# Kernel optimization log

Hardware: AMD Instinct MI355X
Metric: run time of the kernel (lower is better)

## Reference

```python
import jax, jax.numpy as jnp
import numpy as np

B, H, S, D = 2, 16, 2048, 64
DEGREE = 2
EPS = 1e-4


def setup_inputs() -> dict:
    key = jax.random.key(0)
    kq, kk, kv = jax.random.split(key, 3)
    q = jax.random.normal(kq, (B, H, S, D), dtype=jnp.float32)
    k = jax.random.normal(kk, (B, H, S, D), dtype=jnp.float32)
    v = jax.random.normal(kv, (B, H, S, D), dtype=jnp.float32)
    return {"q": q, "k": k, "v": v}


def reference(q, k, v):
    # dots: [B,H,S,S] = QK^T
    dots = jnp.einsum("bhsd,bhtd->bhst", q, k)
    # polynomial kernel: x^degree, row-normalized with clamped denom
    x = dots ** DEGREE
    denom = jnp.maximum(x.sum(axis=-1, keepdims=True), EPS)
    attn = x / denom
    # weighted V sum: [B,H,S,D]
    return jnp.einsum("bhst,bhtd->bhsd", attn, v)
```

## Files before the change

### kernel.cpp

```cpp
#include <hip/hip_runtime.h>


#define S_LEN 2048
#define DH    64
#define BQ    64
#define BK    64
#define EPSTR 68
#define PSTR  65
#define BH_N  32
#define PER_BH (S_LEN * DH)
#define NT    (S_LEN / BK)

typedef __bf16 bf16x8 __attribute__((ext_vector_type(8)));
typedef __bf16 bf16x2 __attribute__((ext_vector_type(2)));
typedef float  f32x4  __attribute__((ext_vector_type(4)));
typedef float  f32x16 __attribute__((ext_vector_type(16)));
typedef unsigned int uivec2 __attribute__((ext_vector_type(2)));

__device__ __forceinline__ unsigned short f2bf(float f) {
    union { float f; unsigned int u; } x; x.f = f;
    unsigned int u = x.u;
    return (unsigned short)((u + 0x7fffu + ((u >> 16) & 1u)) >> 16);
}

__device__ __forceinline__ unsigned int pack2bf(float lo, float hi) {
#if __has_builtin(__builtin_amdgcn_cvt_pk_bf16_f32)
    bf16x2 p = __builtin_amdgcn_cvt_pk_bf16_f32(lo, hi);
    union { bf16x2 v; unsigned int u; } c; c.v = p;
    return c.u;
#else
    return (unsigned int)f2bf(lo) | ((unsigned int)f2bf(hi) << 16);
#endif
}

__device__ __forceinline__ void pl32swap(unsigned int& a, unsigned int& b) {
#if __has_builtin(__builtin_amdgcn_permlane32_swap)
    uivec2 r = __builtin_amdgcn_permlane32_swap(a, b, false, false);
    a = r[0]; b = r[1];
#else
    asm("v_permlane32_swap_b32 %0, %1" : "+v"(a), "+v"(b));
#endif
}

__global__ __launch_bounds__(256)
void prepass_kernel(const float* __restrict__ kg, const float* __restrict__ vg,
                    unsigned short* __restrict__ kfo, unsigned short* __restrict__ vfo)
{
    __shared__ unsigned short Lk[64 * 72];
    __shared__ unsigned short Lv[64 * PSTR];
    const int tid = threadIdx.x;
    const int bh  = blockIdx.y;
    const int t   = blockIdx.x;
    const size_t base = (size_t)bh * PER_BH + (size_t)t * 64 * DH;

    const float4* kf4 = (const float4*)(kg + base);
    const float4* vf4 = (const float4*)(vg + base);
    #pragma unroll
    for (int r = 0; r < 4; ++r) {
        int idx = r * 256 + tid;
        int row = idx >> 4, c4 = idx & 15;
        float4 f = kf4[idx];
        ushort4 hh;
        hh.x = f2bf(f.x); hh.y = f2bf(f.y); hh.z = f2bf(f.z); hh.w = f2bf(f.w);
        *(ushort4*)&Lk[row * 72 + c4 * 4] = hh;
        float4 g = vf4[idx];
        unsigned short* pv = &Lv[row * PSTR + c4 * 4];
        pv[0] = f2bf(g.x); pv[1] = f2bf(g.y); pv[2] = f2bf(g.z); pv[3] = f2bf(g.w);
    }
    __syncthreads();

    unsigned short* kout = kfo + (size_t)bh * PER_BH + (size_t)t * 4096;
    #pragma unroll
    for (int r = 0; r < 2; ++r) {
        int pos = r * 256 + tid;
        int lam = pos & 63, rest = pos >> 6;
        int e = rest >> 2, ks = rest & 3;
        int l31 = lam & 31, h = lam >> 5;
        uint4 v = *(const uint4*)&Lk[(e * 32 + l31) * 72 + ks * 16 + h * 8];
        *(uint4*)(kout + (size_t)pos * 8) = v;
    }
    unsigned short* vout = vfo + (size_t)bh * PER_BH + (size_t)t * 4096;
    #pragma unroll
    for (int r = 0; r < 2; ++r) {
        int pos = r * 256 + tid;
        int lam = pos & 63, rest = pos >> 6;
        int e = rest >> 2, ksl = (rest >> 1) & 1, mt = rest & 1;
        int l31 = lam & 31, h = lam >> 5;
        int d  = mt * 32 + l31;
        int j0 = e * 32 + ksl * 16 + h * 8;
        union { unsigned short s[8]; uint4 u; } u;
        #pragma unroll
        for (int jj = 0; jj < 8; ++jj) u.s[jj] = Lv[(j0 + jj) * PSTR + d];
        *(uint4*)(vout + (size_t)pos * 8) = u.u;
    }
}

__global__ __launch_bounds__(256, 4)
void poly_attn_main(const float* __restrict__ qg,
                    const unsigned short* __restrict__ kfo,
                    const unsigned short* __restrict__ vfo,
                    float* __restrict__ og)
{
    __shared__ float epb[4 * 32 * EPSTR];
    __shared__ float dbuf[128];

    const int tid  = threadIdx.x;
    const int lane = tid & 63;
    const int w    = tid >> 6;
    const int p    = w >> 1;
    const int e    = w & 1;
    const int l31  = lane & 31;
    const int h    = lane >> 5;

    const int id = blockIdx.x;
    const int bh = (id & 7) * 4 + ((id >> 3) & 3);
    const int qt = id >> 5;
    const int q0 = qt * BQ;

    const float* qb = qg + ((size_t)bh * S_LEN + q0) * DH;
    const unsigned short* kw = kfo + (size_t)bh * PER_BH + e * 2048 + (size_t)lane * 8;
    const unsigned short* vw = vfo + (size_t)bh * PER_BH + e * 2048 + (size_t)lane * 8;
    float* ob = og + ((size_t)bh * S_LEN + q0) * DH;

    bf16x8 qfrag[4];
    #pragma unroll
    for (int ks = 0; ks < 4; ++ks) {
        const float* qp = qb + (32 * p + l31) * DH + ks * 16 + h * 8;
        float4 f0 = *(const float4*)qp;
        float4 f1 = *(const float4*)(qp + 4);
        union { unsigned int d[4]; bf16x8 v; } u;
        u.d[0] = pack2bf(f0.x, f0.y);
        u.d[1] = pack2bf(f0.z, f0.w);
        u.d[2] = pack2bf(f1.x, f1.y);
        u.d[3] = pack2bf(f1.z, f1.w);
        qfrag[ks] = u.v;
    }

    f32x16 oacc[2];
    #pragma unroll
    for (int mt = 0; mt < 2; ++mt)
        #pragma unroll
        for (int r = 0; r < 16; ++r) oacc[mt][r] = 0.f;
    float dsum = 0.f;

    uint4 kbuf[2][4], vbuf[2][4];
    #pragma unroll
    for (int x = 0; x < 4; ++x) {
        kbuf[0][x] = *(const uint4*)(kw + x * 512);
        vbuf[0][x] = *(const uint4*)(vw + x * 512);
    }

#define TILE_BODY(T, KCUR, KNXT, VCUR, VNXT)                                        \
    {                                                                               \
        const int tn_ = ((T) + 1) & 31;                                             \
        const unsigned short* kn_ = kw + (size_t)tn_ * 4096;                        \
        const unsigned short* vn_ = vw + (size_t)tn_ * 4096;                        \
        _Pragma("unroll")                                                           \
        for (int x = 0; x < 4; ++x) {                                               \
            KNXT[x] = *(const uint4*)(kn_ + x * 512);                               \
            VNXT[x] = *(const uint4*)(vn_ + x * 512);                               \
        }                                                                           \
        f32x16 acc;                                                                 \
        _Pragma("unroll")                                                           \
        for (int r = 0; r < 16; ++r) acc[r] = 0.f;                                  \
        _Pragma("unroll")                                                           \
        for (int ks = 0; ks < 4; ++ks) {                                            \
            union { uint4 u; bf16x8 v; } kc; kc.u = KCUR[ks];                       \
            acc = __builtin_amdgcn_mfma_f32_32x32x16_bf16(kc.v, qfrag[ks], acc, 0, 0, 0); \
        }                                                                           \
        unsigned int pk[4][2];                                                      \
        _Pragma("unroll")                                                           \
        for (int g = 0; g < 4; ++g) {                                               \
            float x0 = acc[4*g+0], x1 = acc[4*g+1], x2 = acc[4*g+2], x3 = acc[4*g+3]; \
            x0 *= x0; x1 *= x1; x2 *= x2; x3 *= x3;                                 \
            dsum += (x0 + x1) + (x2 + x3);                                          \
            pk[g][0] = pack2bf(x0, x1);                                             \
            pk[g][1] = pack2bf(x2, x3);                                             \
        }                                                                           \
        _Pragma("unroll")                                                           \
        for (int ksl = 0; ksl < 2; ++ksl) {                                         \
            unsigned int a0 = pk[2*ksl][0], b0 = pk[2*ksl+1][0];                    \
            unsigned int a1 = pk[2*ksl][1], b1 = pk[2*ksl+1][1];                    \
            pl32swap(a0, b0);                                                       \
            pl32swap(a1, b1);                                                       \
            union { unsigned int d[4]; bf16x8 v; } bu;                              \
            bu.d[0] = a0; bu.d[1] = a1; bu.d[2] = b0; bu.d[3] = b1;                 \
            _Pragma("unroll")                                                       \
            for (int mt = 0; mt < 2; ++mt) {                                        \
                union { uint4 u; bf16x8 v; } vv; vv.u = VCUR[ksl * 2 + mt];         \
                oacc[mt] = __builtin_amdgcn_mfma_f32_32x32x16_bf16(vv.v, bu.v, oacc[mt], 0, 0, 0); \
            }                                                                       \
        }                                                                           \
    }

    for (int tp = 0; tp < NT; tp += 2) {
        TILE_BODY(tp,     kbuf[0], kbuf[1], vbuf[0], vbuf[1]);
        TILE_BODY(tp + 1, kbuf[1], kbuf[0], vbuf[1], vbuf[0]);
    }
#undef TILE_BODY

    float wavetot = dsum + __shfl_xor(dsum, 32);

    float* ep = epb + (size_t)w * (32 * EPSTR);
    #pragma unroll
    for (int mt = 0; mt < 2; ++mt) {
        #pragma unroll
        for (int g = 0; g < 4; ++g) {
            f32x4 vv;
            vv[0] = oacc[mt][4*g+0];
            vv[1] = oacc[mt][4*g+1];
            vv[2] = oacc[mt][4*g+2];
            vv[3] = oacc[mt][4*g+3];
            *(f32x4*)&ep[l31 * EPSTR + mt * 32 + 8 * g + 4 * h] = vv;
        }
    }
    if (h == 0) dbuf[w * 32 + l31] = wavetot;
    __syncthreads();

    const float* ep0 = epb + (size_t)(2 * p)     * (32 * EPSTR);
    const float* ep1 = epb + (size_t)(2 * p + 1) * (32 * EPSTR);
    const int lrow = e * 16 + (lane >> 2);
    const float den = dbuf[2 * p * 32 + lrow] + dbuf[(2 * p + 1) * 32 + lrow];
    const float inv = 1.0f / fmaxf(den, 1e-4f);
    #pragma unroll
    for (int it = 0; it < 4; ++it) {
        int d0 = (lane & 3) * 16 + it * 4;
        f32x4 a = *(const f32x4*)&ep0[lrow * EPSTR + d0];
        f32x4 b = *(const f32x4*)&ep1[lrow * EPSTR + d0];
        f32x4 s;
        s[0] = (a[0] + b[0]) * inv;
        s[1] = (a[1] + b[1]) * inv;
        s[2] = (a[2] + b[2]) * inv;
        s[3] = (a[3] + b[3]) * inv;
        *(f32x4*)&ob[(32 * p + lrow) * DH + d0] = s;
    }
}

#define LSTR 72
__global__ __launch_bounds__(256, 2)
void poly_attn_fallback(const float* __restrict__ qg, const float* __restrict__ kg,
                        const float* __restrict__ vg, float* __restrict__ og)
{
    __shared__ unsigned short Qs[64 * LSTR];
    __shared__ unsigned short Ksl[64 * LSTR];
    __shared__ unsigned short Vt[64 * LSTR];
    __shared__ unsigned short Xsl[64 * LSTR];

    const int tid  = threadIdx.x;
    const int lane = tid & 63;
    const int w    = tid >> 6;
    const int c    = lane & 15;
    const int quad = lane >> 4;
    const int i0   = w * 16;

    const int bh = blockIdx.y;
    const int q0 = blockIdx.x * 64;

    const float* qb = qg + ((size_t)bh * S_LEN + q0) * DH;
    const float* kb = kg + (size_t)bh * S_LEN * DH;
    const float* vb = vg + (size_t)bh * S_LEN * DH;
    float*       ob = og + ((size_t)bh * S_LEN + q0) * DH;

    {
        const float4* qf4 = (const float4*)qb;
        #pragma unroll
        for (int r = 0; r < 4; ++r) {
            int idx = r * 256 + tid;
            int row = idx >> 4, c4 = idx & 15;
            float4 f = qf4[idx];
            ushort4 hh;
            hh.x = f2bf(f.x); hh.y = f2bf(f.y); hh.z = f2bf(f.z); hh.w = f2bf(f.w);
            *(ushort4*)&Qs[row * LSTR + c4 * 4] = hh;
        }
    }

    f32x4 oacc[4];
    #pragma unroll
    for (int t = 0; t < 4; ++t) { oacc[t][0]=0.f; oacc[t][1]=0.f; oacc[t][2]=0.f; oacc[t][3]=0.f; }
    float dsum[4] = {0.f, 0.f, 0.f, 0.f};

    for (int t0 = 0; t0 < S_LEN; t0 += 64) {
        __syncthreads();
        {
            const float4* kf4 = (const float4*)(kb + (size_t)t0 * DH);
            const float4* vf4 = (const float4*)(vb + (size_t)t0 * DH);
            #pragma unroll
            for (int r = 0; r < 4; ++r) {
                int idx = r * 256 + tid;
                int row = idx >> 4, c4 = idx & 15;
                float4 f = kf4[idx];
                ushort4 hh;
                hh.x = f2bf(f.x); hh.y = f2bf(f.y); hh.z = f2bf(f.z); hh.w = f2bf(f.w);
                *(ushort4*)&Ksl[row * LSTR + c4 * 4] = hh;
                float4 g = vf4[idx];
                int d0 = c4 * 4;
                Vt[(d0 + 0) * LSTR + row] = f2bf(g.x);
                Vt[(d0 + 1) * LSTR + row] = f2bf(g.y);
                Vt[(d0 + 2) * LSTR + row] = f2bf(g.z);
                Vt[(d0 + 3) * LSTR + row] = f2bf(g.w);
            }
        }
        __syncthreads();

        f32x4 xacc[4];
        #pragma unroll
        for (int t = 0; t < 4; ++t) { xacc[t][0]=0.f; xacc[t][1]=0.f; xacc[t][2]=0.f; xacc[t][3]=0.f; }
        #pragma unroll
        for (int k0 = 0; k0 < 64; k0 += 32) {
            bf16x8 af = *(const bf16x8*)&Qs[(i0 + c) * LSTR + k0 + quad * 8];
            #pragma unroll
            for (int tn = 0; tn < 4; ++tn) {
                bf16x8 bfg = *(const bf16x8*)&Ksl[(tn * 16 + c) * LSTR + k0 + quad * 8];
                xacc[tn] = __builtin_amdgcn_mfma_f32_16x16x32_bf16(af, bfg, xacc[tn], 0, 0, 0);
            }
        }
        #pragma unroll
        for (int tn = 0; tn < 4; ++tn)
            #pragma unroll
            for (int r = 0; r < 4; ++r) {
                float xv = xacc[tn][r];
                float xs = xv * xv;
                dsum[r] += xs;
                Xsl[(i0 + quad * 4 + r) * LSTR + tn * 16 + c] = f2bf(xs);
            }
        __syncthreads();

        #pragma unroll
        for (int k0 = 0; k0 < 64; k0 += 32) {
            bf16x8 af = *(const bf16x8*)&Xsl[(i0 + c) * LSTR + k0 + quad * 8];
            #pragma unroll
            for (int tn = 0; tn < 4; ++tn) {
                bf16x8 bfg = *(const bf16x8*)&Vt[(tn * 16 + c) * LSTR + k0 + quad * 8];
                oacc[tn] = __builtin_amdgcn_mfma_f32_16x16x32_bf16(af, bfg, oacc[tn], 0, 0, 0);
            }
        }
    }

    #pragma unroll
    for (int r = 0; r < 4; ++r) {
        float s = dsum[r];
        s += __shfl_xor(s, 1);
        s += __shfl_xor(s, 2);
        s += __shfl_xor(s, 4);
        s += __shfl_xor(s, 8);
        dsum[r] = 1.0f / fmaxf(s, 1e-4f);
    }
    #pragma unroll
    for (int tn = 0; tn < 4; ++tn)
        #pragma unroll
        for (int r = 0; r < 4; ++r)
            ob[(i0 + quad * 4 + r) * DH + tn * 16 + c] = oacc[tn][r] * dsum[r];
}

extern "C" void kernel_launch(void* const* d_in, const int* in_sizes, int n_in,
                              void* d_out, int out_size, void* d_ws, size_t ws_size,
                              hipStream_t stream) {
    (void)in_sizes; (void)n_in; (void)out_size;
    const float* q = (const float*)d_in[0];
    const float* k = (const float*)d_in[1];
    const float* v = (const float*)d_in[2];
    float* o = (float*)d_out;

    const size_t elems = (size_t)BH_N * PER_BH;
    const size_t need  = 2 * elems * sizeof(unsigned short);

    if (ws_size >= need) {
        unsigned short* kfo = (unsigned short*)d_ws;
        unsigned short* vfo = kfo + elems;
        prepass_kernel<<<dim3(NT, BH_N), 256, 0, stream>>>(k, v, kfo, vfo);
        poly_attn_main<<<dim3(BH_N * S_LEN / BQ), 256, 0, stream>>>(q, kfo, vfo, o);
    } else {
        poly_attn_fallback<<<dim3(S_LEN / 64, BH_N), 256, 0, stream>>>(q, k, v, o);
    }
}
```

Baseline: 142.1 us.

## Double query tile per block so each K/V fragment feeds two MFMA row sets

Each wave now handles two 32-row query sub-tiles, so the block covers 128 queries. Every K and V fragment loaded from global memory is reused for both sub-tiles, which halves K/V traffic per query and roughly doubles MFMA work per load. The squaring and denominator accumulation use 2-wide float vectors, and the epilogue is remapped to reduce eight partial tiles. This costs more registers and twice the LDS, so launch bounds drop to 2 blocks per CU, and the grid halves, which may reduce occupancy and load balance.

New measurement: 134.0 us. -5.7%, faster.

```diff
diff --git a/kernel.cpp b/kernel.cpp
--- a/kernel.cpp
+++ b/kernel.cpp
@@ -3,7 +3,7 @@
 
 #define S_LEN 2048
 #define DH    64
-#define BQ    64
+#define BQ    128
 #define BK    64
 #define EPSTR 68
 #define PSTR  65
@@ -13,6 +13,7 @@
 
 typedef __bf16 bf16x8 __attribute__((ext_vector_type(8)));
 typedef __bf16 bf16x2 __attribute__((ext_vector_type(2)));
+typedef float  f32x2  __attribute__((ext_vector_type(2)));
 typedef float  f32x4  __attribute__((ext_vector_type(4)));
 typedef float  f32x16 __attribute__((ext_vector_type(16)));
 typedef unsigned int uivec2 __attribute__((ext_vector_type(2)));
@@ -95,14 +96,14 @@
     }
 }
 
-__global__ __launch_bounds__(256, 4)
+__global__ __launch_bounds__(256, 2)
 void poly_attn_main(const float* __restrict__ qg,
                     const unsigned short* __restrict__ kfo,
                     const unsigned short* __restrict__ vfo,
                     float* __restrict__ og)
 {
-    __shared__ float epb[4 * 32 * EPSTR];
-    __shared__ float dbuf[128];
+    __shared__ float epb[8 * 32 * EPSTR];
+    __shared__ float dbuf[256];
 
     const int tid  = threadIdx.x;
     const int lane = tid & 63;
@@ -113,7 +114,8 @@
     const int h    = lane >> 5;
 
     const int id = blockIdx.x;
-    const int bh = (id & 7) * 4 + ((id >> 3) & 3);
+    const int r5 = id & 31;
+    const int bh = (r5 & 7) * 4 + (r5 >> 3);
     const int qt = id >> 5;
     const int q0 = qt * BQ;
 
@@ -122,26 +124,32 @@
     const unsigned short* vw = vfo + (size_t)bh * PER_BH + e * 2048 + (size_t)lane * 8;
     float* ob = og + ((size_t)bh * S_LEN + q0) * DH;
 
-    bf16x8 qfrag[4];
-    #pragma unroll
-    for (int ks = 0; ks < 4; ++ks) {
-        const float* qp = qb + (32 * p + l31) * DH + ks * 16 + h * 8;
-        float4 f0 = *(const float4*)qp;
-        float4 f1 = *(const float4*)(qp + 4);
-        union { unsigned int d[4]; bf16x8 v; } u;
-        u.d[0] = pack2bf(f0.x, f0.y);
-        u.d[1] = pack2bf(f0.z, f0.w);
-        u.d[2] = pack2bf(f1.x, f1.y);
-        u.d[3] = pack2bf(f1.z, f1.w);
-        qfrag[ks] = u.v;
-    }
-
-    f32x16 oacc[2];
-    #pragma unroll
-    for (int mt = 0; mt < 2; ++mt)
-        #pragma unroll
-        for (int r = 0; r < 16; ++r) oacc[mt][r] = 0.f;
-    float dsum = 0.f;
+    bf16x8 qfrag[2][4];
+    #pragma unroll
+    for (int s = 0; s < 2; ++s) {
+        #pragma unroll
+        for (int ks = 0; ks < 4; ++ks) {
+            const float* qp = qb + (64 * p + 32 * s + l31) * DH + ks * 16 + h * 8;
+            float4 f0 = *(const float4*)qp;
+            float4 f1 = *(const float4*)(qp + 4);
+            union { unsigned int d[4]; bf16x8 v; } u;
+            u.d[0] = pack2bf(f0.x, f0.y);
+            u.d[1] = pack2bf(f0.z, f0.w);
+            u.d[2] = pack2bf(f1.x, f1.y);
+            u.d[3] = pack2bf(f1.z, f1.w);
+            qfrag[s][ks] = u.v;
+        }
+    }
+
+    f32x16 oacc[2][2];
+    #pragma unroll
+    for (int s = 0; s < 2; ++s)
+        #pragma unroll
+        for (int mt = 0; mt < 2; ++mt)
+            #pragma unroll
+            for (int r = 0; r < 16; ++r) oacc[s][mt][r] = 0.f;
+    f32x2 ds2[2];
+    ds2[0][0]=0.f; ds2[0][1]=0.f; ds2[1][0]=0.f; ds2[1][1]=0.f;
 
     uint4 kbuf[2][4], vbuf[2][4];
     #pragma unroll
@@ -160,35 +168,41 @@
             KNXT[x] = *(const uint4*)(kn_ + x * 512);                               \
             VNXT[x] = *(const uint4*)(vn_ + x * 512);                               \
         }                                                                           \
-        f32x16 acc;                                                                 \
+        f32x16 acc0, acc1;                                                          \
         _Pragma("unroll")                                                           \
-        for (int r = 0; r < 16; ++r) acc[r] = 0.f;                                  \
+        for (int r = 0; r < 16; ++r) { acc0[r] = 0.f; acc1[r] = 0.f; }              \
         _Pragma("unroll")                                                           \
         for (int ks = 0; ks < 4; ++ks) {                                            \
             union { uint4 u; bf16x8 v; } kc; kc.u = KCUR[ks];                       \
-            acc = __builtin_amdgcn_mfma_f32_32x32x16_bf16(kc.v, qfrag[ks], acc, 0, 0, 0); \
-        }                                                                           \
-        unsigned int pk[4][2];                                                      \
-        _Pragma("unroll")                                                           \
-        for (int g = 0; g < 4; ++g) {                                               \
-            float x0 = acc[4*g+0], x1 = acc[4*g+1], x2 = acc[4*g+2], x3 = acc[4*g+3]; \
-            x0 *= x0; x1 *= x1; x2 *= x2; x3 *= x3;                                 \
-            dsum += (x0 + x1) + (x2 + x3);                                          \
-            pk[g][0] = pack2bf(x0, x1);                                             \
-            pk[g][1] = pack2bf(x2, x3);                                             \
+            acc0 = __builtin_amdgcn_mfma_f32_32x32x16_bf16(kc.v, qfrag[0][ks], acc0, 0, 0, 0); \
+            acc1 = __builtin_amdgcn_mfma_f32_32x32x16_bf16(kc.v, qfrag[1][ks], acc1, 0, 0, 0); \
         }                                                                           \
         _Pragma("unroll")                                                           \
-        for (int ksl = 0; ksl < 2; ++ksl) {                                         \
-            unsigned int a0 = pk[2*ksl][0], b0 = pk[2*ksl+1][0];                    \
-            unsigned int a1 = pk[2*ksl][1], b1 = pk[2*ksl+1][1];                    \
-            pl32swap(a0, b0);                                                       \
-            pl32swap(a1, b1);                                                       \
-            union { unsigned int d[4]; bf16x8 v; } bu;                              \
-            bu.d[0] = a0; bu.d[1] = a1; bu.d[2] = b0; bu.d[3] = b1;                 \
+        for (int s = 0; s < 2; ++s) {                                               \
+            unsigned int pk[4][2];                                                  \
             _Pragma("unroll")                                                       \
-            for (int mt = 0; mt < 2; ++mt) {                                        \
-                union { uint4 u; bf16x8 v; } vv; vv.u = VCUR[ksl * 2 + mt];         \
-                oacc[mt] = __builtin_amdgcn_mfma_f32_32x32x16_bf16(vv.v, bu.v, oacc[mt], 0, 0, 0); \
+            for (int g = 0; g < 4; ++g) {                                           \
+                f32x2 v01, v23;                                                     \
+                v01[0] = (s ? acc1 : acc0)[4*g+0]; v01[1] = (s ? acc1 : acc0)[4*g+1]; \
+                v23[0] = (s ? acc1 : acc0)[4*g+2]; v23[1] = (s ? acc1 : acc0)[4*g+3]; \
+                v01 = v01 * v01; v23 = v23 * v23;                                   \
+                ds2[s] += v01; ds2[s] += v23;                                       \
+                pk[g][0] = pack2bf(v01[0], v01[1]);                                 \
+                pk[g][1] = pack2bf(v23[0], v23[1]);                                 \
+            }                                                                       \
+            _Pragma("unroll")                                                       \
+            for (int ksl = 0; ksl < 2; ++ksl) {                                     \
+                unsigned int a0 = pk[2*ksl][0], b0 = pk[2*ksl+1][0];                \
+                unsigned int a1 = pk[2*ksl][1], b1 = pk[2*ksl+1][1];                \
+                pl32swap(a0, b0);                                                   \
+                pl32swap(a1, b1);                                                   \
+                union { unsigned int d[4]; bf16x8 v; } bu;                          \
+                bu.d[0] = a0; bu.d[1] = a1; bu.d[2] = b0; bu.d[3] = b1;             \
+                _Pragma("unroll")                                                   \
+                for (int mt = 0; mt < 2; ++mt) {                                    \
+                    union { uint4 u; bf16x8 v; } vv; vv.u = VCUR[ksl * 2 + mt];     \
+                    oacc[s][mt] = __builtin_amdgcn_mfma_f32_32x32x16_bf16(vv.v, bu.v, oacc[s][mt], 0, 0, 0); \
+                }                                                                   \
             }                                                                       \
         }                                                                           \
     }
@@ -199,40 +213,51 @@
     }
 #undef TILE_BODY
 
-    float wavetot = dsum + __shfl_xor(dsum, 32);
-
-    float* ep = epb + (size_t)w * (32 * EPSTR);
-    #pragma unroll
-    for (int mt = 0; mt < 2; ++mt) {
-        #pragma unroll
-        for (int g = 0; g < 4; ++g) {
-            f32x4 vv;
-            vv[0] = oacc[mt][4*g+0];
-            vv[1] = oacc[mt][4*g+1];
-            vv[2] = oacc[mt][4*g+2];
-            vv[3] = oacc[mt][4*g+3];
-            *(f32x4*)&ep[l31 * EPSTR + mt * 32 + 8 * g + 4 * h] = vv;
-        }
-    }
-    if (h == 0) dbuf[w * 32 + l31] = wavetot;
+    float wavetot[2];
+    #pragma unroll
+    for (int s = 0; s < 2; ++s) {
+        float t = ds2[s][0] + ds2[s][1];
+        wavetot[s] = t + __shfl_xor(t, 32);
+    }
+
+    #pragma unroll
+    for (int s = 0; s < 2; ++s) {
+        float* ep = epb + (size_t)(w * 2 + s) * (32 * EPSTR);
+        #pragma unroll
+        for (int mt = 0; mt < 2; ++mt) {
+            #pragma unroll
+            for (int g = 0; g < 4; ++g) {
+                f32x4 vv;
+                vv[0] = oacc[s][mt][4*g+0];
+                vv[1] = oacc[s][mt][4*g+1];
+                vv[2] = oacc[s][mt][4*g+2];
+                vv[3] = oacc[s][mt][4*g+3];
+                *(f32x4*)&ep[l31 * EPSTR + mt * 32 + 8 * g + 4 * h] = vv;
+            }
+        }
+        if (h == 0) dbuf[(w * 2 + s) * 32 + l31] = wavetot[s];
+    }
     __syncthreads();
 
-    const float* ep0 = epb + (size_t)(2 * p)     * (32 * EPSTR);
-    const float* ep1 = epb + (size_t)(2 * p + 1) * (32 * EPSTR);
-    const int lrow = e * 16 + (lane >> 2);
-    const float den = dbuf[2 * p * 32 + lrow] + dbuf[(2 * p + 1) * 32 + lrow];
+    const int psrc = w >> 1, ssrc = w & 1;
+    const int r0 = (2 * psrc + 0) * 2 + ssrc;
+    const int r1 = (2 * psrc + 1) * 2 + ssrc;
+    const int lr = lane >> 1;
+    const float den = dbuf[r0 * 32 + lr] + dbuf[r1 * 32 + lr];
     const float inv = 1.0f / fmaxf(den, 1e-4f);
-    #pragma unroll
-    for (int it = 0; it < 4; ++it) {
-        int d0 = (lane & 3) * 16 + it * 4;
-        f32x4 a = *(const f32x4*)&ep0[lrow * EPSTR + d0];
-        f32x4 b = *(const f32x4*)&ep1[lrow * EPSTR + d0];
-        f32x4 s;
-        s[0] = (a[0] + b[0]) * inv;
-        s[1] = (a[1] + b[1]) * inv;
-        s[2] = (a[2] + b[2]) * inv;
-        s[3] = (a[3] + b[3]) * inv;
-        *(f32x4*)&ob[(32 * p + lrow) * DH + d0] = s;
+    const float* ea = epb + (size_t)r0 * (32 * EPSTR) + lr * EPSTR;
+    const float* eb = epb + (size_t)r1 * (32 * EPSTR) + lr * EPSTR;
+    #pragma unroll
+    for (int it = 0; it < 8; ++it) {
+        int d0 = (lane & 1) * 32 + it * 4;
+        f32x4 a = *(const f32x4*)&ea[d0];
+        f32x4 b = *(const f32x4*)&eb[d0];
+        f32x4 sm;
+        sm[0] = (a[0] + b[0]) * inv;
+        sm[1] = (a[1] + b[1]) * inv;
+        sm[2] = (a[2] + b[2]) * inv;
+        sm[3] = (a[3] + b[3]) * inv;
+        *(f32x4*)&ob[(32 * w + lr) * DH + d0] = sm;
     }
 }
 
```
